# Optimization experiments

Measured on AMD Instinct MI355X. Metric: run time of the kernel, lower is better.

## Reference

```python
import jax, jax.numpy as jnp
import numpy as np

N_NODES = 10000
N_EDGES = 640000
D_IN, D_HID, D_OUT = 128, 256, 64


def setup_inputs() -> dict:
    key = jax.random.key(0)
    k = jax.random.split(key, 8)
    h = jax.random.normal(k[0], (N_NODES, D_IN), dtype=jnp.float32)
    w = jax.random.uniform(k[1], (N_EDGES, 1), dtype=jnp.float32)
    src = jax.random.randint(k[2], (N_EDGES,), 0, N_NODES, dtype=jnp.int32)
    dst = jax.random.randint(k[3], (N_EDGES,), 0, N_NODES, dtype=jnp.int32)
    W1 = jax.random.normal(k[4], (2 * D_IN, D_HID), dtype=jnp.float32) * (1.0 / np.sqrt(2 * D_IN))
    b1 = jnp.zeros((D_HID,), dtype=jnp.float32)
    W2 = jax.random.normal(k[5], (2 * D_HID, D_OUT), dtype=jnp.float32) * (1.0 / np.sqrt(2 * D_HID))
    b2 = jnp.zeros((D_OUT,), dtype=jnp.float32)
    return {"h": h, "w": w, "src": src, "dst": dst, "W1": W1, "b1": b1, "W2": W2, "b2": b2}


def _sage_layer(h, w, src, dst, W, b, n_nodes):
    # message: m_e = h[src_e] * w_e  (scalar edge weight broadcast over features)
    m = h[src] * w  # [E, D]
    # mean scatter-reduce over incoming edges per destination node
    s = jax.ops.segment_sum(m, dst, num_segments=n_nodes)          # [N, D]
    deg = jax.ops.segment_sum(jnp.ones((dst.shape[0],), h.dtype), dst, num_segments=n_nodes)
    h_N = jnp.where(deg[:, None] > 0, s / jnp.maximum(deg, 1.0)[:, None], 0.0)
    # concat + linear
    return jnp.concatenate([h, h_N], axis=1) @ W + b


def reference(h, w, src, dst, W1, b1, W2, b2):
    n = h.shape[0]
    x = _sage_layer(h, w, src, dst, W1, b1, n)
    x = jax.nn.relu(x)
    return _sage_layer(x, w, src, dst, W2, b2, n)
```

## Files before the change

kernel.cpp:

```cpp
#include <hip/hip_runtime.h>
#include <hip/hip_fp16.h>


#define NSUB 4
#define CAPS 64

typedef _Float16 f16x8 __attribute__((ext_vector_type(8)));
typedef float f32x4 __attribute__((ext_vector_type(4)));


#define FB 2048

__global__ __launch_bounds__(256) void fill_k(const int* __restrict__ src,
                                              const int* __restrict__ dst,
                                              const float* __restrict__ w,
                                              const float* __restrict__ h,
                                              const float* __restrict__ W1,
                                              const float* __restrict__ W2,
                                              int* __restrict__ cursor,
                                              unsigned int* __restrict__ ebuf,
                                              __half* __restrict__ hh,
                                              __half* __restrict__ W1z,
                                              __half* __restrict__ W2z,
                                              int E, int N, int NH4) {
  if (blockIdx.x < FB) {
    const int grp = blockIdx.x & 7;
    const int bi = blockIdx.x >> 3;
    const int nbg = FB >> 3;
    const int chunk = (N + 7) >> 3;
    const int lo = grp * chunk;
    const int hi = min(N, lo + chunk);
    for (int i = bi * 256 + threadIdx.x; i < E; i += nbg * 256) {
      const int d = dst[i];
      if (d >= lo && d < hi) {
        const int sub = i & (NSUB - 1);
        const int p = atomicAdd(&cursor[d * NSUB + sub], 1);
        if (p < CAPS) {
          const __half hw = __float2half_rn(w[i]);
          ebuf[((size_t)(d * NSUB + sub)) * CAPS + p] =
              ((unsigned int)src[i] << 16) | (unsigned int)__half_as_ushort(hw);
        }
      }
    }
    return;
  }
  const int t = (blockIdx.x - FB) * 256 + threadIdx.x;
  if (t < NH4) {
    const float4 v = reinterpret_cast<const float4*>(h)[t];
    reinterpret_cast<__half2*>(hh)[2 * t] = __floats2half2_rn(v.x, v.y);
    reinterpret_cast<__half2*>(hh)[2 * t + 1] = __floats2half2_rn(v.z, v.w);
    return;
  }
  const int tw1 = t - NH4;
  if (tw1 < 8192) {
    const int ln = tw1 & 63;
    const int nt = (tw1 >> 6) & 15;
    const int kc = tw1 >> 10;
    const int kbase = kc * 32 + (ln >> 4) * 8;
    const int n = nt * 16 + (ln & 15);
    __half tmp[8];
#pragma unroll
    for (int j = 0; j < 8; ++j)
      tmp[j] = __float2half_rn(W1[(size_t)(kbase + j) * 256 + n]);
    *reinterpret_cast<uint4*>(W1z + (size_t)tw1 * 8) = *reinterpret_cast<uint4*>(tmp);
    return;
  }
  const int tw2 = tw1 - 8192;
  if (tw2 < 4096) {
    const int ln = tw2 & 63;
    const int nt = (tw2 >> 6) & 7;
    const int kc = tw2 >> 9;
    const int kbase = kc * 32 + (ln >> 4) * 8;
    const int np = nt * 16 + (ln & 15);
    __half tmp[8];
#pragma unroll
    for (int j = 0; j < 8; ++j) {
      const int k = kbase + j;
      const float v = (np < 64) ? W2[(size_t)k * 64 + np]
                                : W2[(size_t)(256 + k) * 64 + (np - 64)];
      tmp[j] = __float2half_rn(v);
    }
    *reinterpret_cast<uint4*>(W2z + (size_t)tw2 * 8) = *reinterpret_cast<uint4*>(tmp);
  }
}

#define ACC8(q, wt)                                              \
  {                                                              \
    const float2 t0 = __half22float2(*(const __half2*)&(q).x);   \
    const float2 t1 = __half22float2(*(const __half2*)&(q).y);   \
    const float2 t2 = __half22float2(*(const __half2*)&(q).z);   \
    const float2 t3 = __half22float2(*(const __half2*)&(q).w);   \
    a[0] += t0.x * (wt); a[1] += t0.y * (wt);                    \
    a[2] += t1.x * (wt); a[3] += t1.y * (wt);                    \
    a[4] += t2.x * (wt); a[5] += t2.y * (wt);                    \
    a[6] += t3.x * (wt); a[7] += t3.y * (wt);                    \
  }


__global__ __launch_bounds__(256) void agg1_k(const __half* __restrict__ hh,
                                              const unsigned int* __restrict__ ebuf,
                                              const int* __restrict__ cnt,
                                              __half* __restrict__ G1, int N) {
  const int chunk = (N + 7) >> 3;
  const int g8 = blockIdx.x & 7;
  const int k = blockIdx.x >> 3;
  const int wv = threadIdx.x >> 6;
  const int node_sel = wv >> 1;
  const int half = wv & 1;
  const int loc = k * 2 + node_sel;
  const int n = g8 * chunk + loc;
  const int lane = threadIdx.x & 63;
  const int g = lane >> 4;
  const int f = lane & 15;
  const uint4* __restrict__ H = reinterpret_cast<const uint4*>(hh);
  __shared__ float part[2][2][16][8];
  __shared__ int degs[2][2];
  float a[8] = {};
  int deg = 0;
  const bool valid = (loc < chunk) && (n < N);
  if (valid) {
#pragma unroll
    for (int s = 0; s < 2; ++s) {
      const int seg = half * 2 + s;
      const int m = min(cnt[n * NSUB + seg], CAPS);
      deg += m;
      const unsigned int* __restrict__ bkt =
          ebuf + ((size_t)(n * NSUB + seg)) * CAPS;
      const unsigned int pk = (lane < m) ? bkt[lane] : 0u;
      int j = 0;
      for (; j + 7 < m; j += 8) {
        const unsigned int pA = __shfl(pk, j + g);
        const unsigned int pB = __shfl(pk, j + 4 + g);
        const float wA = __half2float(__ushort_as_half((unsigned short)pA));
        const float wB = __half2float(__ushort_as_half((unsigned short)pB));
        const uint4 qA = H[(size_t)(pA >> 16) * 16 + f];
        const uint4 qB = H[(size_t)(pB >> 16) * 16 + f];
        ACC8(qA, wA)
        ACC8(qB, wB)
      }
      for (; j < m; j += 4) {
        const int jj = j + g;
        const unsigned int p = __shfl(pk, jj < m ? jj : (m - 1));
        float wt = __half2float(__ushort_as_half((unsigned short)p));
        if (jj >= m) wt = 0.f;
        const uint4 q = H[(size_t)(p >> 16) * 16 + f];
        ACC8(q, wt)
      }
    }
  }
#pragma unroll
  for (int r = 0; r < 8; ++r) {
    a[r] += __shfl_xor(a[r], 16);
    a[r] += __shfl_xor(a[r], 32);
  }
  if (lane < 16) {
#pragma unroll
    for (int r = 0; r < 8; ++r) part[node_sel][half][f][r] = a[r];
    if (f == 0) degs[node_sel][half] = deg;
  }
  __syncthreads();
  if (half == 0 && lane < 16 && valid) {
    const int d = degs[node_sel][0] + degs[node_sel][1];
    const float inv = (d > 0) ? 1.0f / (float)d : 0.0f;
    __half tmp[8];
#pragma unroll
    for (int r = 0; r < 8; ++r)
      tmp[r] = __float2half_rn((part[node_sel][0][f][r] + part[node_sel][1][f][r]) * inv);
    reinterpret_cast<uint4*>(G1)[(size_t)n * 16 + f] = *reinterpret_cast<uint4*>(tmp);
  }
}


__global__ __launch_bounds__(256) void gemm1zu_k(const __half* __restrict__ hh,
                                                 const __half* __restrict__ G1,
                                                 const __half* __restrict__ W1z,
                                                 const float* __restrict__ b1,
                                                 const __half* __restrict__ W2z,
                                                 __half* __restrict__ Z,
                                                 float* __restrict__ U) {
  const int tid = threadIdx.x;
  const int w = tid >> 6, lane = tid & 63;
  const int m0 = blockIdx.x * 16;
  const int row_in = m0 + (lane & 15);
  const int qoff = (lane >> 4) * 8;
  const int colq = lane & 15;
  const int rowq = (lane >> 4) * 4;

  f32x4 acc[4] = {};
  const __half* __restrict__ Ah = hh + (size_t)row_in * 128;
  const __half* __restrict__ Ag = G1 + (size_t)row_in * 128;
#pragma unroll
  for (int kc = 0; kc < 8; ++kc) {
    const __half* asrc = (kc < 4) ? (Ah + kc * 32 + qoff) : (Ag + (kc - 4) * 32 + qoff);
    const f16x8 af = *reinterpret_cast<const f16x8*>(asrc);
    const __half* bbase = W1z + ((size_t)(kc * 16 + w * 4) * 64 + lane) * 8;
#pragma unroll
    for (int nt = 0; nt < 4; ++nt) {
      const f16x8 bf = *reinterpret_cast<const f16x8*>(bbase + (size_t)nt * 64 * 8);
      acc[nt] = __builtin_amdgcn_mfma_f32_16x16x32_f16(af, bf, acc[nt], 0, 0, 0);
    }
  }
  __shared__ alignas(16) __half Hs[16][264];
#pragma unroll
  for (int nt = 0; nt < 4; ++nt) {
    const int col = w * 64 + nt * 16 + colq;
    const float bz = b1[col];
#pragma unroll
    for (int r = 0; r < 4; ++r)
      Hs[rowq + r][col] = __float2half_rn(fmaxf(acc[nt][r] + bz, 0.f));
  }
  __syncthreads();

  f32x4 accz[2] = {};
#pragma unroll
  for (int kc = 0; kc < 8; ++kc) {
    const f16x8 af = *reinterpret_cast<const f16x8*>(&Hs[lane & 15][kc * 32 + qoff]);
    const __half* bbase = W2z + ((size_t)(kc * 8 + w * 2) * 64 + lane) * 8;
#pragma unroll
    for (int nt = 0; nt < 2; ++nt) {
      const f16x8 bf = *reinterpret_cast<const f16x8*>(bbase + (size_t)nt * 64 * 8);
      accz[nt] = __builtin_amdgcn_mfma_f32_16x16x32_f16(af, bf, accz[nt], 0, 0, 0);
    }
  }
  __shared__ float S[16][132];
#pragma unroll
  for (int nt = 0; nt < 2; ++nt) {
    const int col = w * 32 + nt * 16 + colq;
#pragma unroll
    for (int r = 0; r < 4; ++r) S[rowq + r][col] = accz[nt][r];
  }
  __syncthreads();
  {
    const int row = tid >> 4, c4 = tid & 15;
    const float4 v = make_float4(S[row][c4 * 4], S[row][c4 * 4 + 1],
                                 S[row][c4 * 4 + 2], S[row][c4 * 4 + 3]);
    *reinterpret_cast<float4*>(&U[(size_t)(m0 + row) * 64 + c4 * 4]) = v;
  }
  if (tid < 128) {
    const int row = tid >> 3, c8 = tid & 7;
    const float* s = &S[row][64 + c8 * 8];
    const __half2 h0 = __floats2half2_rn(s[0], s[1]);
    const __half2 h1 = __floats2half2_rn(s[2], s[3]);
    const __half2 h2 = __floats2half2_rn(s[4], s[5]);
    const __half2 h3 = __floats2half2_rn(s[6], s[7]);
    uint4 q;
    q.x = *reinterpret_cast<const unsigned int*>(&h0);
    q.y = *reinterpret_cast<const unsigned int*>(&h1);
    q.z = *reinterpret_cast<const unsigned int*>(&h2);
    q.w = *reinterpret_cast<const unsigned int*>(&h3);
    *reinterpret_cast<uint4*>(&Z[(size_t)(m0 + row) * 64 + c8 * 8]) = q;
  }
}


__global__ __launch_bounds__(256) void agg2z_k(const __half* __restrict__ Z,
                                               const float* __restrict__ U,
                                               const float* __restrict__ b2,
                                               const unsigned int* __restrict__ ebuf,
                                               const int* __restrict__ cnt,
                                               float* __restrict__ out, int N) {
  const int chunk = (N + 7) >> 3;
  const int g8 = blockIdx.x & 7;
  const int k = blockIdx.x >> 3;
  const int loc = k * 4 + (threadIdx.x >> 6);
  const int n = g8 * chunk + loc;
  if (loc >= chunk || n >= N) return;
  const int lane = threadIdx.x & 63;
  const int g = lane >> 3;
  const int f = lane & 7;
  const uint4* __restrict__ Zr = reinterpret_cast<const uint4*>(Z);
  float a[8] = {};
  int deg = 0;
#pragma unroll
  for (int seg = 0; seg < NSUB; ++seg) {
    const int m = min(cnt[n * NSUB + seg], CAPS);
    deg += m;
    const unsigned int* __restrict__ bkt = ebuf + ((size_t)(n * NSUB + seg)) * CAPS;
    const unsigned int pk = (lane < m) ? bkt[lane] : 0u;
    int j = 0;
    for (; j + 15 < m; j += 16) {
      const unsigned int pA = __shfl(pk, j + g);
      const unsigned int pB = __shfl(pk, j + 8 + g);
      const float wA = __half2float(__ushort_as_half((unsigned short)pA));
      const float wB = __half2float(__ushort_as_half((unsigned short)pB));
      const uint4 qA = Zr[(size_t)(pA >> 16) * 8 + f];
      const uint4 qB = Zr[(size_t)(pB >> 16) * 8 + f];
      ACC8(qA, wA)
      ACC8(qB, wB)
    }
    for (; j < m; j += 8) {
      const int jj = j + g;
      const unsigned int p = __shfl(pk, jj < m ? jj : (m - 1));
      float wt = __half2float(__ushort_as_half((unsigned short)p));
      if (jj >= m) wt = 0.f;
      const uint4 q = Zr[(size_t)(p >> 16) * 8 + f];
      ACC8(q, wt)
    }
  }
#pragma unroll
  for (int r = 0; r < 8; ++r) {
    a[r] += __shfl_xor(a[r], 8);
    a[r] += __shfl_xor(a[r], 16);
    a[r] += __shfl_xor(a[r], 32);
  }
  if (lane < 8) {
    const float inv = (deg > 0) ? 1.0f / (float)deg : 0.0f;
    const float4 u0 = *reinterpret_cast<const float4*>(&U[(size_t)n * 64 + f * 8]);
    const float4 u1 = *reinterpret_cast<const float4*>(&U[(size_t)n * 64 + f * 8 + 4]);
    const float4 z0 = *reinterpret_cast<const float4*>(&b2[f * 8]);
    const float4 z1 = *reinterpret_cast<const float4*>(&b2[f * 8 + 4]);
    float4 o0, o1;
    o0.x = a[0] * inv + u0.x + z0.x;
    o0.y = a[1] * inv + u0.y + z0.y;
    o0.z = a[2] * inv + u0.z + z0.z;
    o0.w = a[3] * inv + u0.w + z0.w;
    o1.x = a[4] * inv + u1.x + z1.x;
    o1.y = a[5] * inv + u1.y + z1.y;
    o1.z = a[6] * inv + u1.z + z1.z;
    o1.w = a[7] * inv + u1.w + z1.w;
    *reinterpret_cast<float4*>(&out[(size_t)n * 64 + f * 8]) = o0;
    *reinterpret_cast<float4*>(&out[(size_t)n * 64 + f * 8 + 4]) = o1;
  }
}


extern "C" void kernel_launch(void* const* d_in, const int* in_sizes, int n_in,
                              void* d_out, int out_size, void* d_ws, size_t ws_size,
                              hipStream_t stream) {
  const float* h   = (const float*)d_in[0];
  const float* w   = (const float*)d_in[1];
  const int*   src = (const int*)d_in[2];
  const int*   dst = (const int*)d_in[3];
  const float* W1  = (const float*)d_in[4];
  const float* b1  = (const float*)d_in[5];
  const float* W2  = (const float*)d_in[6];
  const float* b2  = (const float*)d_in[7];
  float* out = (float*)d_out;

  const int N = in_sizes[0] / 128;
  const int E = in_sizes[2];

  char* ws = (char*)d_ws;
  size_t o = 0;
  auto alloc = [&](size_t bytes) -> void* {
    void* p = ws + o;
    o = (o + bytes + 255) & ~(size_t)255;
    return p;
  };
  int*          cursor = (int*)alloc((size_t)N * NSUB * 4);
  unsigned int* ebuf   = (unsigned int*)alloc((size_t)N * NSUB * CAPS * 4);
  __half*       hh     = (__half*)alloc((size_t)N * 128 * 2);
  __half*       G1     = (__half*)alloc((size_t)N * 128 * 2);
  __half*       Z      = (__half*)alloc((size_t)N * 64 * 2);
  float*        U      = (float*)alloc((size_t)N * 64 * 4);
  __half*       W1z    = (__half*)alloc((size_t)256 * 256 * 2);
  __half*       W2z    = (__half*)alloc((size_t)256 * 128 * 2);

  const int NH4 = N * 32;
  const int prep_blocks = (NH4 + 8192 + 4096 + 255) / 256;
  const int chunk = (N + 7) >> 3;

  hipMemsetAsync(cursor, 0, (size_t)N * NSUB * 4, stream);
  fill_k<<<FB + prep_blocks, 256, 0, stream>>>(src, dst, w, h, W1, W2, cursor,
                                               ebuf, hh, W1z, W2z, E, N, NH4);
  agg1_k<<<8 * ((chunk + 1) / 2), 256, 0, stream>>>(hh, ebuf, cursor, G1, N);
  gemm1zu_k<<<N / 16, 256, 0, stream>>>(hh, G1, W1z, b1, W2z, Z, U);
  agg2z_k<<<8 * ((chunk + 3) / 4), 256, 0, stream>>>(Z, U, b2, ebuf, cursor, out, N);
}
```

Measured before the change: 143.6 us.

## Fuse layer-1 aggregation into the GEMM kernel via shared-memory G1 tile

The separate layer-1 mean-aggregation kernel is merged into the first GEMM kernel. Each block now aggregates its own 16 nodes, one wave handling four nodes sequentially across all four sub-buckets, and stages the averaged features in shared memory instead of writing and re-reading a global G1 buffer. This removes one launch and the G1 round trip to global memory. In exchange there is less parallelism per node during aggregation, each wave walks its nodes serially, and the grid is only N/16 blocks, so the memory-latency-bound gather may be hidden less well. The tail reads of 10000/16 blocks also assume N divides by 16, as before.

```diff
diff --git a/kernel.cpp b/kernel.cpp
--- a/kernel.cpp
+++ b/kernel.cpp
@@ -4,12 +4,11 @@
 
 #define NSUB 4
 #define CAPS 64
+#define FB 2048
 
 typedef _Float16 f16x8 __attribute__((ext_vector_type(8)));
 typedef float f32x4 __attribute__((ext_vector_type(4)));
 
-
-#define FB 2048
 
 __global__ __launch_bounds__(256) void fill_k(const int* __restrict__ src,
                                               const int* __restrict__ dst,
@@ -97,113 +96,96 @@
   }
 
 
-__global__ __launch_bounds__(256) void agg1_k(const __half* __restrict__ hh,
-                                              const unsigned int* __restrict__ ebuf,
-                                              const int* __restrict__ cnt,
-                                              __half* __restrict__ G1, int N) {
-  const int chunk = (N + 7) >> 3;
-  const int g8 = blockIdx.x & 7;
-  const int k = blockIdx.x >> 3;
-  const int wv = threadIdx.x >> 6;
-  const int node_sel = wv >> 1;
-  const int half = wv & 1;
-  const int loc = k * 2 + node_sel;
-  const int n = g8 * chunk + loc;
-  const int lane = threadIdx.x & 63;
-  const int g = lane >> 4;
-  const int f = lane & 15;
-  const uint4* __restrict__ H = reinterpret_cast<const uint4*>(hh);
-  __shared__ float part[2][2][16][8];
-  __shared__ int degs[2][2];
-  float a[8] = {};
-  int deg = 0;
-  const bool valid = (loc < chunk) && (n < N);
-  if (valid) {
-#pragma unroll
-    for (int s = 0; s < 2; ++s) {
-      const int seg = half * 2 + s;
-      const int m = min(cnt[n * NSUB + seg], CAPS);
-      deg += m;
-      const unsigned int* __restrict__ bkt =
-          ebuf + ((size_t)(n * NSUB + seg)) * CAPS;
-      const unsigned int pk = (lane < m) ? bkt[lane] : 0u;
-      int j = 0;
-      for (; j + 7 < m; j += 8) {
-        const unsigned int pA = __shfl(pk, j + g);
-        const unsigned int pB = __shfl(pk, j + 4 + g);
-        const float wA = __half2float(__ushort_as_half((unsigned short)pA));
-        const float wB = __half2float(__ushort_as_half((unsigned short)pB));
-        const uint4 qA = H[(size_t)(pA >> 16) * 16 + f];
-        const uint4 qB = H[(size_t)(pB >> 16) * 16 + f];
-        ACC8(qA, wA)
-        ACC8(qB, wB)
-      }
-      for (; j < m; j += 4) {
-        const int jj = j + g;
-        const unsigned int p = __shfl(pk, jj < m ? jj : (m - 1));
-        float wt = __half2float(__ushort_as_half((unsigned short)p));
-        if (jj >= m) wt = 0.f;
-        const uint4 q = H[(size_t)(p >> 16) * 16 + f];
-        ACC8(q, wt)
-      }
-    }
-  }
-#pragma unroll
-  for (int r = 0; r < 8; ++r) {
-    a[r] += __shfl_xor(a[r], 16);
-    a[r] += __shfl_xor(a[r], 32);
-  }
-  if (lane < 16) {
-#pragma unroll
-    for (int r = 0; r < 8; ++r) part[node_sel][half][f][r] = a[r];
-    if (f == 0) degs[node_sel][half] = deg;
-  }
-  __syncthreads();
-  if (half == 0 && lane < 16 && valid) {
-    const int d = degs[node_sel][0] + degs[node_sel][1];
-    const float inv = (d > 0) ? 1.0f / (float)d : 0.0f;
-    __half tmp[8];
-#pragma unroll
-    for (int r = 0; r < 8; ++r)
-      tmp[r] = __float2half_rn((part[node_sel][0][f][r] + part[node_sel][1][f][r]) * inv);
-    reinterpret_cast<uint4*>(G1)[(size_t)n * 16 + f] = *reinterpret_cast<uint4*>(tmp);
-  }
-}
-
-
-__global__ __launch_bounds__(256) void gemm1zu_k(const __half* __restrict__ hh,
-                                                 const __half* __restrict__ G1,
+__global__ __launch_bounds__(256) void gemmagg_k(const __half* __restrict__ hh,
+                                                 const unsigned int* __restrict__ ebuf,
+                                                 const int* __restrict__ cnt,
                                                  const __half* __restrict__ W1z,
                                                  const float* __restrict__ b1,
                                                  const __half* __restrict__ W2z,
                                                  __half* __restrict__ Z,
                                                  float* __restrict__ U) {
   const int tid = threadIdx.x;
-  const int w = tid >> 6, lane = tid & 63;
+  const int wv = tid >> 6, lane = tid & 63;
   const int m0 = blockIdx.x * 16;
-  const int row_in = m0 + (lane & 15);
+  __shared__ alignas(16) __half G1s[16][136];
+  __shared__ alignas(16) __half Hs[16][264];
+  __shared__ float S[16][132];
+
+  {
+    const int g = lane >> 4;
+    const int f = lane & 15;
+    const uint4* __restrict__ H = reinterpret_cast<const uint4*>(hh);
+#pragma unroll
+    for (int q = 0; q < 4; ++q) {
+      const int local = wv * 4 + q;
+      const int n = m0 + local;
+      float a[8] = {};
+      int deg = 0;
+#pragma unroll
+      for (int seg = 0; seg < NSUB; ++seg) {
+        const int m = min(cnt[n * NSUB + seg], CAPS);
+        deg += m;
+        const unsigned int* __restrict__ bkt =
+            ebuf + ((size_t)(n * NSUB + seg)) * CAPS;
+        const unsigned int pk = (lane < m) ? bkt[lane] : 0u;
+        int j = 0;
+        for (; j + 7 < m; j += 8) {
+          const unsigned int pA = __shfl(pk, j + g);
+          const unsigned int pB = __shfl(pk, j + 4 + g);
+          const float wA = __half2float(__ushort_as_half((unsigned short)pA));
+          const float wB = __half2float(__ushort_as_half((unsigned short)pB));
+          const uint4 qA = H[(size_t)(pA >> 16) * 16 + f];
+          const uint4 qB = H[(size_t)(pB >> 16) * 16 + f];
+          ACC8(qA, wA)
+          ACC8(qB, wB)
+        }
+        for (; j < m; j += 4) {
+          const int jj = j + g;
+          const unsigned int p = __shfl(pk, jj < m ? jj : (m - 1));
+          float wt = __half2float(__ushort_as_half((unsigned short)p));
+          if (jj >= m) wt = 0.f;
+          const uint4 qv = H[(size_t)(p >> 16) * 16 + f];
+          ACC8(qv, wt)
+        }
+      }
+#pragma unroll
+      for (int r = 0; r < 8; ++r) {
+        a[r] += __shfl_xor(a[r], 16);
+        a[r] += __shfl_xor(a[r], 32);
+      }
+      if (lane < 16) {
+        const float inv = (deg > 0) ? 1.0f / (float)deg : 0.0f;
+        __half tmp[8];
+#pragma unroll
+        for (int r = 0; r < 8; ++r) tmp[r] = __float2half_rn(a[r] * inv);
+        *reinterpret_cast<uint4*>(&G1s[local][f * 8]) =
+            *reinterpret_cast<uint4*>(tmp);
+      }
+    }
+  }
+  __syncthreads();
+
+  const int row16 = lane & 15;
   const int qoff = (lane >> 4) * 8;
   const int colq = lane & 15;
   const int rowq = (lane >> 4) * 4;
-
   f32x4 acc[4] = {};
-  const __half* __restrict__ Ah = hh + (size_t)row_in * 128;
-  const __half* __restrict__ Ag = G1 + (size_t)row_in * 128;
+  const __half* __restrict__ Ah = hh + (size_t)(m0 + row16) * 128;
 #pragma unroll
   for (int kc = 0; kc < 8; ++kc) {
-    const __half* asrc = (kc < 4) ? (Ah + kc * 32 + qoff) : (Ag + (kc - 4) * 32 + qoff);
+    const __half* asrc =
+        (kc < 4) ? (Ah + kc * 32 + qoff) : (&G1s[row16][(kc - 4) * 32 + qoff]);
     const f16x8 af = *reinterpret_cast<const f16x8*>(asrc);
-    const __half* bbase = W1z + ((size_t)(kc * 16 + w * 4) * 64 + lane) * 8;
+    const __half* bbase = W1z + ((size_t)(kc * 16 + wv * 4) * 64 + lane) * 8;
 #pragma unroll
     for (int nt = 0; nt < 4; ++nt) {
       const f16x8 bf = *reinterpret_cast<const f16x8*>(bbase + (size_t)nt * 64 * 8);
       acc[nt] = __builtin_amdgcn_mfma_f32_16x16x32_f16(af, bf, acc[nt], 0, 0, 0);
     }
   }
-  __shared__ alignas(16) __half Hs[16][264];
 #pragma unroll
   for (int nt = 0; nt < 4; ++nt) {
-    const int col = w * 64 + nt * 16 + colq;
+    const int col = wv * 64 + nt * 16 + colq;
     const float bz = b1[col];
 #pragma unroll
     for (int r = 0; r < 4; ++r)
@@ -214,18 +196,17 @@
   f32x4 accz[2] = {};
 #pragma unroll
   for (int kc = 0; kc < 8; ++kc) {
-    const f16x8 af = *reinterpret_cast<const f16x8*>(&Hs[lane & 15][kc * 32 + qoff]);
-    const __half* bbase = W2z + ((size_t)(kc * 8 + w * 2) * 64 + lane) * 8;
+    const f16x8 af = *reinterpret_cast<const f16x8*>(&Hs[row16][kc * 32 + qoff]);
+    const __half* bbase = W2z + ((size_t)(kc * 8 + wv * 2) * 64 + lane) * 8;
 #pragma unroll
     for (int nt = 0; nt < 2; ++nt) {
       const f16x8 bf = *reinterpret_cast<const f16x8*>(bbase + (size_t)nt * 64 * 8);
       accz[nt] = __builtin_amdgcn_mfma_f32_16x16x32_f16(af, bf, accz[nt], 0, 0, 0);
     }
   }
-  __shared__ float S[16][132];
 #pragma unroll
   for (int nt = 0; nt < 2; ++nt) {
-    const int col = w * 32 + nt * 16 + colq;
+    const int col = wv * 32 + nt * 16 + colq;
 #pragma unroll
     for (int r = 0; r < 4; ++r) S[rowq + r][col] = accz[nt][r];
   }
@@ -350,7 +331,6 @@
   int*          cursor = (int*)alloc((size_t)N * NSUB * 4);
   unsigned int* ebuf   = (unsigned int*)alloc((size_t)N * NSUB * CAPS * 4);
   __half*       hh     = (__half*)alloc((size_t)N * 128 * 2);
-  __half*       G1     = (__half*)alloc((size_t)N * 128 * 2);
   __half*       Z      = (__half*)alloc((size_t)N * 64 * 2);
   float*        U      = (float*)alloc((size_t)N * 64 * 4);
   __half*       W1z    = (__half*)alloc((size_t)256 * 256 * 2);
@@ -363,7 +343,6 @@
   hipMemsetAsync(cursor, 0, (size_t)N * NSUB * 4, stream);
   fill_k<<<FB + prep_blocks, 256, 0, stream>>>(src, dst, w, h, W1, W2, cursor,
                                                ebuf, hh, W1z, W2z, E, N, NH4);
-  agg1_k<<<8 * ((chunk + 1) / 2), 256, 0, stream>>>(hh, ebuf, cursor, G1, N);
-  gemm1zu_k<<<N / 16, 256, 0, stream>>>(hh, G1, W1z, b1, W2z, Z, U);
+  gemmagg_k<<<N / 16, 256, 0, stream>>>(hh, ebuf, cursor, W1z, b1, W2z, Z, U);
   agg2z_k<<<8 * ((chunk + 3) / 4), 256, 0, stream>>>(Z, U, b2, ebuf, cursor, out, N);
 }
```

After: 151.0 us. 5.2% more time.
